# Kernel tuning notes

Measured on AMD Instinct MI355X. Metric: run time of the kernel, lower is better.

## Reference

```python
import jax, jax.numpy as jnp
import numpy as np

N = 100000
E = 1600000
IN_C, HID_C, OUT_C = 128, 128, 64
EPS = 1e-5


def setup_inputs() -> dict:
    key = jax.random.key(0)
    ks = jax.random.split(key, 12)
    x = jax.random.normal(ks[0], (N, IN_C), dtype=jnp.float32)
    edge_index = jax.random.randint(ks[1], (2, E), 0, N, dtype=jnp.int64)
    def lin(k, fan_in, fan_out):
        s = 1.0 / np.sqrt(fan_in)
        return jax.random.uniform(k, (fan_in, fan_out), jnp.float32, -s, s)
    return {
        "x": x,
        "W1": lin(ks[2], IN_C, HID_C), "b1": jnp.zeros((HID_C,), jnp.float32),
        "g1": jnp.ones((HID_C,), jnp.float32), "be1": jnp.zeros((HID_C,), jnp.float32),
        "W2": lin(ks[3], HID_C, HID_C), "b2": jnp.zeros((HID_C,), jnp.float32),
        "g2": jnp.ones((HID_C,), jnp.float32), "be2": jnp.zeros((HID_C,), jnp.float32),
        "W3": lin(ks[4], HID_C, OUT_C), "b3": jnp.zeros((OUT_C,), jnp.float32),
        "edge_index": edge_index,
    }


def gcn_conv(x, W, b, src, dst, dinv):
    # x' = D^{-1/2}(A+I)D^{-1/2} (x W) + b ; src/dst already include self loops
    h = x @ W                                    # [N, C_out]
    norm = dinv[src] * dinv[dst]                 # [E+N]
    msg = h[src] * norm[:, None]                 # [E+N, C_out] (memory-bound gather)
    out = jax.ops.segment_sum(msg, dst, num_segments=N)
    return out + b


def batchnorm_relu(h, gamma, beta):
    # training-mode BatchNorm1d: batch stats over nodes, biased variance
    mean = jnp.mean(h, axis=0)
    var = jnp.mean((h - mean) ** 2, axis=0)
    y = gamma * (h - mean) * jax.lax.rsqrt(var + EPS) + beta
    return jax.nn.relu(y)


def reference(x, W1, b1, g1, be1, W2, b2, g2, be2, W3, b3, edge_index):
    loop = jnp.arange(N, dtype=edge_index.dtype)
    src = jnp.concatenate([edge_index[0], loop])
    dst = jnp.concatenate([edge_index[1], loop])
    deg = jax.ops.segment_sum(jnp.ones_like(dst, dtype=jnp.float32), dst, num_segments=N)
    dinv = jax.lax.rsqrt(jnp.maximum(deg, 1.0))

    h = gcn_conv(x, W1, b1, src, dst, dinv)
    h = batchnorm_relu(h, g1, be1)
    h = gcn_conv(h, W2, b2, src, dst, dinv)
    h = batchnorm_relu(h, g2, be2)
    out = gcn_conv(h, W3, b3, src, dst, dinv)
    return (h, out)
```

## Files before the change

### kernel.cpp

```cpp
#include <hip/hip_runtime.h>
#include <hip/hip_bf16.h>

#define NNODES 100000
#define NEDGES 1600000
#define EPSBN 1e-5f

#define BKT_SHIFT 9
#define NODES_PER_BKT 512
#define NBKT 196
#define NCHUNK 256
#define CHUNK 6250
#define SRC_MASK 0x1FFFF
#define NSLOT 64

typedef unsigned short u16;
typedef unsigned int u32;
typedef __bf16 bf16x8 __attribute__((ext_vector_type(8)));
typedef float floatx4 __attribute__((ext_vector_type(4)));

__device__ __forceinline__ u16 f2bf(float f) {
    unsigned int u = __float_as_uint(f);
    unsigned int r = (u + 0x7fffu + ((u >> 16) & 1u)) >> 16;
    return (u16)r;
}
__device__ __forceinline__ float bflo(unsigned int u) { return __uint_as_float(u << 16); }
__device__ __forceinline__ float bfhi(unsigned int u) { return __uint_as_float(u & 0xffff0000u); }


__global__ __launch_bounds__(256) void k_hist(const int* __restrict__ ei, int* __restrict__ histT) {
    __shared__ int h[NBKT];
    int tid = threadIdx.x;
    if (tid < NBKT) h[tid] = 0;
    __syncthreads();
    int base = blockIdx.x * CHUNK;
    for (int e = base + tid; e < base + CHUNK; e += 256) {
        int d = ei[NEDGES + e];
        atomicAdd(&h[d >> BKT_SHIFT], 1);
    }
    __syncthreads();
    if (tid < NBKT) histT[tid * NCHUNK + blockIdx.x] = h[tid];
}

__global__ __launch_bounds__(256) void k_bbase(const int* __restrict__ histT, int* __restrict__ bbase,
                                               int* __restrict__ rowptr) {
    __shared__ int sdata[256];
    int tid = threadIdx.x;
    int s = 0;
    if (tid < NBKT) {
        for (int g = 0; g < NCHUNK; ++g) s += histT[tid * NCHUNK + g];
    }
    int val = s;
    sdata[tid] = val;
    __syncthreads();
    for (int off = 1; off < 256; off <<= 1) {
        int add = (tid >= off) ? sdata[tid - off] : 0;
        __syncthreads();
        val += add;
        sdata[tid] = val;
        __syncthreads();
    }
    if (tid < NBKT) bbase[tid] = val - s;
    if (tid == 0) { bbase[NBKT] = NEDGES; rowptr[NNODES] = NEDGES; }
}

__global__ __launch_bounds__(256) void k_bscan(const int* __restrict__ histT, const int* __restrict__ bbase,
                                               int* __restrict__ offT) {
    __shared__ int sdata[256];
    int b = blockIdx.x;
    int g = threadIdx.x;
    int v = histT[b * NCHUNK + g];
    int val = v;
    sdata[g] = val;
    __syncthreads();
    for (int off = 1; off < 256; off <<= 1) {
        int add = (g >= off) ? sdata[g - off] : 0;
        __syncthreads();
        val += add;
        sdata[g] = val;
        __syncthreads();
    }
    offT[b * NCHUNK + g] = bbase[b] + (val - v);
}

__global__ __launch_bounds__(256) void k_scatter(const int* __restrict__ ei, const int* __restrict__ offT,
                                                 u32* __restrict__ rec) {
    __shared__ int cur[NBKT];
    int tid = threadIdx.x;
    if (tid < NBKT) cur[tid] = offT[tid * NCHUNK + blockIdx.x];
    __syncthreads();
    int base = blockIdx.x * CHUNK;
    for (int e = base + tid; e < base + CHUNK; e += 256) {
        int s = ei[e];
        int d = ei[NEDGES + e];
        int b = d >> BKT_SHIFT;
        int p = atomicAdd(&cur[b], 1);
        rec[p] = ((u32)(d & (NODES_PER_BKT - 1)) << 17) | (u32)s;
    }
}

__global__ __launch_bounds__(256) void k_bfill(const u32* __restrict__ rec, const int* __restrict__ bbase,
                                               int* __restrict__ rowptr, float* __restrict__ dinv,
                                               int* __restrict__ colsrc) {
    __shared__ int cnt[NODES_PER_BKT];
    __shared__ int sdata[256];
    int tid = threadIdx.x;
    int b = blockIdx.x;
    int n0 = b * NODES_PER_BKT;
    int r0 = bbase[b], r1 = bbase[b + 1];
    cnt[2 * tid] = 0;
    cnt[2 * tid + 1] = 0;
    __syncthreads();
    for (int r = r0 + tid; r < r1; r += 256) {
        atomicAdd(&cnt[rec[r] >> 17], 1);
    }
    __syncthreads();
    int c0 = cnt[2 * tid], c1 = cnt[2 * tid + 1];
    int ps = c0 + c1;
    int val = ps;
    sdata[tid] = val;
    __syncthreads();
    for (int off = 1; off < 256; off <<= 1) {
        int add = (tid >= off) ? sdata[tid - off] : 0;
        __syncthreads();
        val += add;
        sdata[tid] = val;
        __syncthreads();
    }
    int e0 = val - ps;
    int e1 = e0 + c0;
    int na = n0 + 2 * tid, nb2 = n0 + 2 * tid + 1;
    if (na < NNODES) {
        rowptr[na] = r0 + e0;
        dinv[na] = rsqrtf((float)(c0 + 1));
    }
    if (nb2 < NNODES) {
        rowptr[nb2] = r0 + e1;
        dinv[nb2] = rsqrtf((float)(c1 + 1));
    }
    cnt[2 * tid] = r0 + e0;
    cnt[2 * tid + 1] = r0 + e1;
    __syncthreads();
    for (int r = r0 + tid; r < r1; r += 256) {
        u32 u = rec[r];
        int p = atomicAdd(&cnt[u >> 17], 1);
        colsrc[p] = (int)(u & SRC_MASK);
    }
}


template <int COUT>
__device__ __forceinline__ void packone(const float* __restrict__ W, u16* __restrict__ Wp, int f) {
    constexpr int CT = COUT / 16;
    if (f >= 4 * CT * 64) return;
    int ks = f / (CT * 64);
    int ct = (f / 64) % CT;
    int lane = f % 64;
    int quad = lane >> 4, mm = lane & 15;
#pragma unroll
    for (int j = 0; j < 8; ++j) {
        float v = W[(size_t)(ks * 32 + quad * 8 + j) * COUT + ct * 16 + mm];
        Wp[(size_t)f * 8 + j] = f2bf(v);
    }
}

__global__ __launch_bounds__(256) void k_packW_all(const float* __restrict__ W1, const float* __restrict__ W2,
                                                   const float* __restrict__ W3, u16* __restrict__ Wp1,
                                                   u16* __restrict__ Wp2, u16* __restrict__ Wp3) {
    int b = blockIdx.x;
    if (b < 8) packone<128>(W1, Wp1, b * 256 + threadIdx.x);
    else if (b < 16) packone<128>(W2, Wp2, (b - 8) * 256 + threadIdx.x);
    else packone<64>(W3, Wp3, (b - 16) * 256 + threadIdx.x);
}


template <int COUT, bool AFFINE, bool WRITEH>
__global__ __launch_bounds__(256) void k_mfma_gemm(const float* __restrict__ Xf, const u16* __restrict__ Wp,
                                                   const float* __restrict__ dinv,
                                                   const float* __restrict__ scale, const float* __restrict__ shift,
                                                   u16* __restrict__ Bout, float* __restrict__ Hout) {
    constexpr int CT = COUT / 16;
    const int wave = threadIdx.x >> 6;
    const int lane = threadIdx.x & 63;
    const int quad = lane >> 4;
    const int m = lane & 15;
    const int rowbase = blockIdx.x * 64 + wave * 16;
    const int arow = rowbase + m;
    const bool rv = arow < NNODES;
    floatx4 acc[CT];
#pragma unroll
    for (int ct = 0; ct < CT; ++ct) acc[ct] = floatx4{0.f, 0.f, 0.f, 0.f};
#pragma unroll
    for (int ks = 0; ks < 4; ++ks) {
        const int k0 = ks * 32 + quad * 8;
        float4 xa = make_float4(0.f, 0.f, 0.f, 0.f), xb = xa;
        if (rv) {
            xa = *(const float4*)(Xf + (size_t)arow * 128 + k0);
            xb = *(const float4*)(Xf + (size_t)arow * 128 + k0 + 4);
        }
        if (AFFINE) {
            float4 sa = *(const float4*)(scale + k0), sb = *(const float4*)(scale + k0 + 4);
            float4 ha = *(const float4*)(shift + k0), hb = *(const float4*)(shift + k0 + 4);
            xa.x = fmaxf(fmaf(xa.x, sa.x, ha.x), 0.f);
            xa.y = fmaxf(fmaf(xa.y, sa.y, ha.y), 0.f);
            xa.z = fmaxf(fmaf(xa.z, sa.z, ha.z), 0.f);
            xa.w = fmaxf(fmaf(xa.w, sa.w, ha.w), 0.f);
            xb.x = fmaxf(fmaf(xb.x, sb.x, hb.x), 0.f);
            xb.y = fmaxf(fmaf(xb.y, sb.y, hb.y), 0.f);
            xb.z = fmaxf(fmaf(xb.z, sb.z, hb.z), 0.f);
            xb.w = fmaxf(fmaf(xb.w, sb.w, hb.w), 0.f);
        }
        if (WRITEH && rv) {
            *(float4*)(Hout + (size_t)arow * 128 + k0) = xa;
            *(float4*)(Hout + (size_t)arow * 128 + k0 + 4) = xb;
        }
        union { u16 h[8]; bf16x8 v; } ua;
        ua.h[0] = f2bf(xa.x); ua.h[1] = f2bf(xa.y); ua.h[2] = f2bf(xa.z); ua.h[3] = f2bf(xa.w);
        ua.h[4] = f2bf(xb.x); ua.h[5] = f2bf(xb.y); ua.h[6] = f2bf(xb.z); ua.h[7] = f2bf(xb.w);
#pragma unroll
        for (int ct = 0; ct < CT; ++ct) {
            uint4 bv = *(const uint4*)(Wp + ((size_t)(ks * CT + ct) * 64 + lane) * 8);
            bf16x8 b = *(const bf16x8*)&bv;
            acc[ct] = __builtin_amdgcn_mfma_f32_16x16x32_bf16(ua.v, b, acc[ct], 0, 0, 0);
        }
    }
    float dv[4];
#pragma unroll
    for (int reg = 0; reg < 4; ++reg) {
        int r = rowbase + quad * 4 + reg;
        dv[reg] = (r < NNODES) ? dinv[r] : 0.f;
    }
#pragma unroll
    for (int ct = 0; ct < CT; ++ct) {
#pragma unroll
        for (int reg = 0; reg < 4; ++reg) {
            int r = rowbase + quad * 4 + reg;
            if (r < NNODES) Bout[(size_t)r * COUT + ct * 16 + m] = f2bf(dv[reg] * acc[ct][reg]);
        }
    }
}


template <bool STATS>
__global__ __launch_bounds__(256) void k_agg128v(const u16* __restrict__ Bm, const float* __restrict__ dinv,
                                                 const int* __restrict__ rowptr, const int* __restrict__ colsrc,
                                                 const float* __restrict__ bias, float* __restrict__ Out,
                                                 float* __restrict__ slots) {
    __shared__ float sO[4][128];
    const int wave = threadIdx.x >> 6;
    const int node = blockIdx.x * 4 + wave;
    const int lane = threadIdx.x & 63;
    const int g = lane >> 4;
    const int c16 = lane & 15;
    const uint4* Bq = (const uint4*)Bm;
    float a0[8], a1[8];
#pragma unroll
    for (int j = 0; j < 8; ++j) { a0[j] = 0.f; a1[j] = 0.f; }
    const int beg = rowptr[node];
    const int L = rowptr[node + 1] - beg + 1;
    for (int it = 0; it < L; it += 8) {
        int i0 = it + g, i1 = it + 4 + g;
        float w0 = (i0 < L) ? 1.f : 0.f;
        float w1 = (i1 < L) ? 1.f : 0.f;
        i0 = min(i0, L - 1);
        i1 = min(i1, L - 1);
        int s0 = colsrc[beg + max(i0, 1) - 1];
        int s1 = colsrc[beg + max(i1, 1) - 1];
        if (i0 == 0) s0 = node;
        uint4 q0 = Bq[(size_t)s0 * 16 + c16];
        uint4 q1 = Bq[(size_t)s1 * 16 + c16];
        a0[0] += w0 * bflo(q0.x); a0[1] += w0 * bfhi(q0.x);
        a0[2] += w0 * bflo(q0.y); a0[3] += w0 * bfhi(q0.y);
        a0[4] += w0 * bflo(q0.z); a0[5] += w0 * bfhi(q0.z);
        a0[6] += w0 * bflo(q0.w); a0[7] += w0 * bfhi(q0.w);
        a1[0] += w1 * bflo(q1.x); a1[1] += w1 * bfhi(q1.x);
        a1[2] += w1 * bflo(q1.y); a1[3] += w1 * bfhi(q1.y);
        a1[4] += w1 * bflo(q1.z); a1[5] += w1 * bfhi(q1.z);
        a1[6] += w1 * bflo(q1.w); a1[7] += w1 * bfhi(q1.w);
    }
    const float dv = dinv[node];
    float o[8];
#pragma unroll
    for (int j = 0; j < 8; ++j) {
        float s = a0[j] + a1[j];
        s += __shfl_xor(s, 16);
        s += __shfl_xor(s, 32);
        o[j] = dv * s + bias[c16 * 8 + j];
    }
    if (g == 0) {
        float4 v0 = make_float4(o[0], o[1], o[2], o[3]);
        float4 v1 = make_float4(o[4], o[5], o[6], o[7]);
        *(float4*)(Out + (size_t)node * 128 + c16 * 8) = v0;
        *(float4*)(Out + (size_t)node * 128 + c16 * 8 + 4) = v1;
        if (STATS) {
#pragma unroll
            for (int j = 0; j < 8; ++j) sO[wave][c16 * 8 + j] = o[j];
        }
    }
    if (STATS) {
        __syncthreads();
        if (threadIdx.x < 128) {
            float s = 0.f, q = 0.f;
#pragma unroll
            for (int wv = 0; wv < 4; ++wv) {
                float v = sO[wv][threadIdx.x];
                s += v;
                q += v * v;
            }
            float* slot = slots + (size_t)(blockIdx.x & (NSLOT - 1)) * 256;
            atomicAdd(&slot[threadIdx.x], s);
            atomicAdd(&slot[128 + threadIdx.x], q);
        }
    }
}

__global__ __launch_bounds__(256) void k_agg64v(const u16* __restrict__ Bm, const float* __restrict__ dinv,
                                                const int* __restrict__ rowptr, const int* __restrict__ colsrc,
                                                const float* __restrict__ bias, float* __restrict__ Out) {
    const int node = blockIdx.x * 4 + (threadIdx.x >> 6);
    const int lane = threadIdx.x & 63;
    const int g = lane >> 3;
    const int c8 = lane & 7;
    const uint4* Bq = (const uint4*)Bm;
    float a0[8], a1[8];
#pragma unroll
    for (int j = 0; j < 8; ++j) { a0[j] = 0.f; a1[j] = 0.f; }
    const int beg = rowptr[node];
    const int L = rowptr[node + 1] - beg + 1;
    for (int it = 0; it < L; it += 16) {
        int i0 = it + g, i1 = it + 8 + g;
        float w0 = (i0 < L) ? 1.f : 0.f;
        float w1 = (i1 < L) ? 1.f : 0.f;
        i0 = min(i0, L - 1);
        i1 = min(i1, L - 1);
        int s0 = colsrc[beg + max(i0, 1) - 1];
        int s1 = colsrc[beg + max(i1, 1) - 1];
        if (i0 == 0) s0 = node;
        uint4 q0 = Bq[(size_t)s0 * 8 + c8];
        uint4 q1 = Bq[(size_t)s1 * 8 + c8];
        a0[0] += w0 * bflo(q0.x); a0[1] += w0 * bfhi(q0.x);
        a0[2] += w0 * bflo(q0.y); a0[3] += w0 * bfhi(q0.y);
        a0[4] += w0 * bflo(q0.z); a0[5] += w0 * bfhi(q0.z);
        a0[6] += w0 * bflo(q0.w); a0[7] += w0 * bfhi(q0.w);
        a1[0] += w1 * bflo(q1.x); a1[1] += w1 * bfhi(q1.x);
        a1[2] += w1 * bflo(q1.y); a1[3] += w1 * bfhi(q1.y);
        a1[4] += w1 * bflo(q1.z); a1[5] += w1 * bfhi(q1.z);
        a1[6] += w1 * bflo(q1.w); a1[7] += w1 * bfhi(q1.w);
    }
    const float dv = dinv[node];
    float o[8];
#pragma unroll
    for (int j = 0; j < 8; ++j) {
        float s = a0[j] + a1[j];
        s += __shfl_xor(s, 8);
        s += __shfl_xor(s, 16);
        s += __shfl_xor(s, 32);
        o[j] = dv * s + bias[c8 * 8 + j];
    }
    if (g == 0) {
        float4 v0 = make_float4(o[0], o[1], o[2], o[3]);
        float4 v1 = make_float4(o[4], o[5], o[6], o[7]);
        *(float4*)(Out + (size_t)node * 64 + c8 * 8) = v0;
        *(float4*)(Out + (size_t)node * 64 + c8 * 8 + 4) = v1;
    }
}


__global__ void k_bn_final(const float* __restrict__ slots, const float* __restrict__ g,
                           const float* __restrict__ be, float* __restrict__ scale, float* __restrict__ shift) {
    int c = threadIdx.x;
    float s = 0.f, q = 0.f;
    for (int k = 0; k < NSLOT; ++k) {
        s += slots[(size_t)k * 256 + c];
        q += slots[(size_t)k * 256 + 128 + c];
    }
    float mean = s * (1.0f / NNODES);
    float var = q * (1.0f / NNODES) - mean * mean;
    float istd = rsqrtf(var + EPSBN);
    float sc = g[c] * istd;
    scale[c] = sc;
    shift[c] = be[c] - sc * mean;
}


extern "C" void kernel_launch(void* const* d_in, const int* in_sizes, int n_in,
                              void* d_out, int out_size, void* d_ws, size_t ws_size,
                              hipStream_t stream) {
    const float* x   = (const float*)d_in[0];
    const float* W1  = (const float*)d_in[1];
    const float* b1  = (const float*)d_in[2];
    const float* g1  = (const float*)d_in[3];
    const float* be1 = (const float*)d_in[4];
    const float* W2  = (const float*)d_in[5];
    const float* b2  = (const float*)d_in[6];
    const float* g2  = (const float*)d_in[7];
    const float* be2 = (const float*)d_in[8];
    const float* W3  = (const float*)d_in[9];
    const float* b3  = (const float*)d_in[10];
    const int* ei    = (const int*)d_in[11];

    float* out_h = (float*)d_out;
    float* out_o = (float*)d_out + (size_t)NNODES * 128;

    char* w = (char*)d_ws;
    float* A = (float*)w;      w += (size_t)NNODES * 128 * 4;
    u16* Bm = (u16*)w;         w += (size_t)NNODES * 128 * 2;
    float* dinv = (float*)w;   w += (size_t)NNODES * 4;
    int* rowptr = (int*)w;     w += (size_t)(NNODES + 32) * 4;
    int* colsrc = (int*)w;     w += (size_t)(NEDGES + 8) * 4;
    int* bbase = (int*)w;      w += (NBKT + 4) * 4;
    float* slots1 = (float*)w; w += (size_t)NSLOT * 256 * 4;
    float* slots2 = (float*)w; w += (size_t)NSLOT * 256 * 4;
    float* scale = (float*)w;  w += 128 * 4;
    float* shift = (float*)w;  w += 128 * 4;
    u16* Wp1 = (u16*)w;        w += 128 * 128 * 2;
    u16* Wp2 = (u16*)w;        w += 128 * 128 * 2;
    u16* Wp3 = (u16*)w;        w += 128 * 64 * 2;

    u32* rec  = (u32*)A;
    int* histT = (int*)Bm;
    int* offT  = (int*)Bm + NBKT * NCHUNK;

    hipMemsetAsync(slots1, 0, (size_t)2 * NSLOT * 256 * 4, stream);

    k_packW_all<<<20, 256, 0, stream>>>(W1, W2, W3, Wp1, Wp2, Wp3);

    k_hist<<<NCHUNK, 256, 0, stream>>>(ei, histT);
    k_bbase<<<1, 256, 0, stream>>>(histT, bbase, rowptr);
    k_bscan<<<NBKT, 256, 0, stream>>>(histT, bbase, offT);
    k_scatter<<<NCHUNK, 256, 0, stream>>>(ei, offT, rec);
    k_bfill<<<NBKT, 256, 0, stream>>>(rec, bbase, rowptr, dinv, colsrc);

    const int GB = (NNODES + 63) / 64;
    const int AB = NNODES / 4;

    k_mfma_gemm<128, false, false><<<GB, 256, 0, stream>>>(x, Wp1, dinv, nullptr, nullptr, Bm, nullptr);
    k_agg128v<true><<<AB, 256, 0, stream>>>(Bm, dinv, rowptr, colsrc, b1, A, slots1);
    k_bn_final<<<1, 128, 0, stream>>>(slots1, g1, be1, scale, shift);

    k_mfma_gemm<128, true, false><<<GB, 256, 0, stream>>>(A, Wp2, dinv, scale, shift, Bm, nullptr);
    k_agg128v<true><<<AB, 256, 0, stream>>>(Bm, dinv, rowptr, colsrc, b2, A, slots2);
    k_bn_final<<<1, 128, 0, stream>>>(slots2, g2, be2, scale, shift);

    k_mfma_gemm<64, true, true><<<GB, 256, 0, stream>>>(A, Wp3, dinv, scale, shift, Bm, out_h);
    k_agg64v<<<AB, 256, 0, stream>>>(Bm, dinv, rowptr, colsrc, b3, out_o);
}
```

Before: 460.4 us.

## Slab-partition features into 16-channel slabs so aggregation gathers fit in cache

The GEMM writes its bf16 output in a channel-slab layout of 16 channels by all nodes. The aggregation kernels now run one block per (node group, slab), so each gather pass touches only one slab of about 3.2 MB that can stay cache-resident. Intermediate activations are now stored as bf16 slabs instead of fp32, which halves their traffic. BN stats now use per-node atomics rather than a per-block shared-memory reduction, which adds more atomic contention, and the extra bf16 rounding of activations changes precision.

```diff
diff --git a/kernel.cpp b/kernel.cpp
--- a/kernel.cpp
+++ b/kernel.cpp
@@ -173,8 +173,8 @@
 }
 
 
-template <int COUT, bool AFFINE, bool WRITEH>
-__global__ __launch_bounds__(256) void k_mfma_gemm(const float* __restrict__ Xf, const u16* __restrict__ Wp,
+template <int COUT, bool BF16A, bool AFFINE, bool WRITEH>
+__global__ __launch_bounds__(256) void k_mfma_gemm(const void* __restrict__ Xin, const u16* __restrict__ Wp,
                                                    const float* __restrict__ dinv,
                                                    const float* __restrict__ scale, const float* __restrict__ shift,
                                                    u16* __restrict__ Bout, float* __restrict__ Hout) {
@@ -192,30 +192,45 @@
 #pragma unroll
     for (int ks = 0; ks < 4; ++ks) {
         const int k0 = ks * 32 + quad * 8;
-        float4 xa = make_float4(0.f, 0.f, 0.f, 0.f), xb = xa;
-        if (rv) {
-            xa = *(const float4*)(Xf + (size_t)arow * 128 + k0);
-            xb = *(const float4*)(Xf + (size_t)arow * 128 + k0 + 4);
+        float xv[8];
+        if (BF16A) {
+            uint4 q = make_uint4(0u, 0u, 0u, 0u);
+            if (rv) {
+                const u16* base = (const u16*)Xin + ((size_t)((k0 >> 4) * NNODES + arow)) * 16 + (k0 & 15);
+                q = *(const uint4*)base;
+            }
+            xv[0] = bflo(q.x); xv[1] = bfhi(q.x);
+            xv[2] = bflo(q.y); xv[3] = bfhi(q.y);
+            xv[4] = bflo(q.z); xv[5] = bfhi(q.z);
+            xv[6] = bflo(q.w); xv[7] = bfhi(q.w);
+        } else {
+            float4 xa = make_float4(0.f, 0.f, 0.f, 0.f), xb = xa;
+            if (rv) {
+                xa = *(const float4*)((const float*)Xin + (size_t)arow * 128 + k0);
+                xb = *(const float4*)((const float*)Xin + (size_t)arow * 128 + k0 + 4);
+            }
+            xv[0] = xa.x; xv[1] = xa.y; xv[2] = xa.z; xv[3] = xa.w;
+            xv[4] = xb.x; xv[5] = xb.y; xv[6] = xb.z; xv[7] = xb.w;
         }
         if (AFFINE) {
             float4 sa = *(const float4*)(scale + k0), sb = *(const float4*)(scale + k0 + 4);
             float4 ha = *(const float4*)(shift + k0), hb = *(const float4*)(shift + k0 + 4);
-            xa.x = fmaxf(fmaf(xa.x, sa.x, ha.x), 0.f);
-            xa.y = fmaxf(fmaf(xa.y, sa.y, ha.y), 0.f);
-            xa.z = fmaxf(fmaf(xa.z, sa.z, ha.z), 0.f);
-            xa.w = fmaxf(fmaf(xa.w, sa.w, ha.w), 0.f);
-            xb.x = fmaxf(fmaf(xb.x, sb.x, hb.x), 0.f);
-            xb.y = fmaxf(fmaf(xb.y, sb.y, hb.y), 0.f);
-            xb.z = fmaxf(fmaf(xb.z, sb.z, hb.z), 0.f);
-            xb.w = fmaxf(fmaf(xb.w, sb.w, hb.w), 0.f);
+            xv[0] = fmaxf(fmaf(xv[0], sa.x, ha.x), 0.f);
+            xv[1] = fmaxf(fmaf(xv[1], sa.y, ha.y), 0.f);
+            xv[2] = fmaxf(fmaf(xv[2], sa.z, ha.z), 0.f);
+            xv[3] = fmaxf(fmaf(xv[3], sa.w, ha.w), 0.f);
+            xv[4] = fmaxf(fmaf(xv[4], sb.x, hb.x), 0.f);
+            xv[5] = fmaxf(fmaf(xv[5], sb.y, hb.y), 0.f);
+            xv[6] = fmaxf(fmaf(xv[6], sb.z, hb.z), 0.f);
+            xv[7] = fmaxf(fmaf(xv[7], sb.w, hb.w), 0.f);
         }
         if (WRITEH && rv) {
-            *(float4*)(Hout + (size_t)arow * 128 + k0) = xa;
-            *(float4*)(Hout + (size_t)arow * 128 + k0 + 4) = xb;
+            *(float4*)(Hout + (size_t)arow * 128 + k0) = make_float4(xv[0], xv[1], xv[2], xv[3]);
+            *(float4*)(Hout + (size_t)arow * 128 + k0 + 4) = make_float4(xv[4], xv[5], xv[6], xv[7]);
         }
         union { u16 h[8]; bf16x8 v; } ua;
-        ua.h[0] = f2bf(xa.x); ua.h[1] = f2bf(xa.y); ua.h[2] = f2bf(xa.z); ua.h[3] = f2bf(xa.w);
-        ua.h[4] = f2bf(xb.x); ua.h[5] = f2bf(xb.y); ua.h[6] = f2bf(xb.z); ua.h[7] = f2bf(xb.w);
+#pragma unroll
+        for (int j = 0; j < 8; ++j) ua.h[j] = f2bf(xv[j]);
 #pragma unroll
         for (int ct = 0; ct < CT; ++ct) {
             uint4 bv = *(const uint4*)(Wp + ((size_t)(ks * CT + ct) * 64 + lane) * 8);
@@ -234,133 +249,107 @@
 #pragma unroll
         for (int reg = 0; reg < 4; ++reg) {
             int r = rowbase + quad * 4 + reg;
-            if (r < NNODES) Bout[(size_t)r * COUT + ct * 16 + m] = f2bf(dv[reg] * acc[ct][reg]);
+            if (r < NNODES) Bout[((size_t)(ct * NNODES + r)) * 16 + m] = f2bf(dv[reg] * acc[ct][reg]);
         }
     }
 }
 
 
 template <bool STATS>
-__global__ __launch_bounds__(256) void k_agg128v(const u16* __restrict__ Bm, const float* __restrict__ dinv,
+__global__ __launch_bounds__(256) void k_aggs128(const u16* __restrict__ Bs, const float* __restrict__ dinv,
                                                  const int* __restrict__ rowptr, const int* __restrict__ colsrc,
-                                                 const float* __restrict__ bias, float* __restrict__ Out,
+                                                 const float* __restrict__ bias, u16* __restrict__ As,
                                                  float* __restrict__ slots) {
-    __shared__ float sO[4][128];
+    const int slab = blockIdx.x & 7;
     const int wave = threadIdx.x >> 6;
-    const int node = blockIdx.x * 4 + wave;
-    const int lane = threadIdx.x & 63;
-    const int g = lane >> 4;
-    const int c16 = lane & 15;
-    const uint4* Bq = (const uint4*)Bm;
-    float a0[8], a1[8];
-#pragma unroll
-    for (int j = 0; j < 8; ++j) { a0[j] = 0.f; a1[j] = 0.f; }
-    const int beg = rowptr[node];
-    const int L = rowptr[node + 1] - beg + 1;
-    for (int it = 0; it < L; it += 8) {
-        int i0 = it + g, i1 = it + 4 + g;
-        float w0 = (i0 < L) ? 1.f : 0.f;
-        float w1 = (i1 < L) ? 1.f : 0.f;
-        i0 = min(i0, L - 1);
-        i1 = min(i1, L - 1);
-        int s0 = colsrc[beg + max(i0, 1) - 1];
-        int s1 = colsrc[beg + max(i1, 1) - 1];
-        if (i0 == 0) s0 = node;
-        uint4 q0 = Bq[(size_t)s0 * 16 + c16];
-        uint4 q1 = Bq[(size_t)s1 * 16 + c16];
-        a0[0] += w0 * bflo(q0.x); a0[1] += w0 * bfhi(q0.x);
-        a0[2] += w0 * bflo(q0.y); a0[3] += w0 * bfhi(q0.y);
-        a0[4] += w0 * bflo(q0.z); a0[5] += w0 * bfhi(q0.z);
-        a0[6] += w0 * bflo(q0.w); a0[7] += w0 * bfhi(q0.w);
-        a1[0] += w1 * bflo(q1.x); a1[1] += w1 * bfhi(q1.x);
-        a1[2] += w1 * bflo(q1.y); a1[3] += w1 * bfhi(q1.y);
-        a1[4] += w1 * bflo(q1.z); a1[5] += w1 * bfhi(q1.z);
-        a1[6] += w1 * bflo(q1.w); a1[7] += w1 * bfhi(q1.w);
-    }
-    const float dv = dinv[node];
-    float o[8];
-#pragma unroll
-    for (int j = 0; j < 8; ++j) {
-        float s = a0[j] + a1[j];
-        s += __shfl_xor(s, 16);
-        s += __shfl_xor(s, 32);
-        o[j] = dv * s + bias[c16 * 8 + j];
-    }
-    if (g == 0) {
-        float4 v0 = make_float4(o[0], o[1], o[2], o[3]);
-        float4 v1 = make_float4(o[4], o[5], o[6], o[7]);
-        *(float4*)(Out + (size_t)node * 128 + c16 * 8) = v0;
-        *(float4*)(Out + (size_t)node * 128 + c16 * 8 + 4) = v1;
-        if (STATS) {
-#pragma unroll
-            for (int j = 0; j < 8; ++j) sO[wave][c16 * 8 + j] = o[j];
-        }
-    }
-    if (STATS) {
-        __syncthreads();
-        if (threadIdx.x < 128) {
-            float s = 0.f, q = 0.f;
-#pragma unroll
-            for (int wv = 0; wv < 4; ++wv) {
-                float v = sO[wv][threadIdx.x];
-                s += v;
-                q += v * v;
-            }
-            float* slot = slots + (size_t)(blockIdx.x & (NSLOT - 1)) * 256;
-            atomicAdd(&slot[threadIdx.x], s);
-            atomicAdd(&slot[128 + threadIdx.x], q);
-        }
-    }
-}
-
-__global__ __launch_bounds__(256) void k_agg64v(const u16* __restrict__ Bm, const float* __restrict__ dinv,
-                                                const int* __restrict__ rowptr, const int* __restrict__ colsrc,
-                                                const float* __restrict__ bias, float* __restrict__ Out) {
-    const int node = blockIdx.x * 4 + (threadIdx.x >> 6);
+    const int node = (blockIdx.x >> 3) * 4 + wave;
     const int lane = threadIdx.x & 63;
     const int g = lane >> 3;
     const int c8 = lane & 7;
-    const uint4* Bq = (const uint4*)Bm;
-    float a0[8], a1[8];
-#pragma unroll
-    for (int j = 0; j < 8; ++j) { a0[j] = 0.f; a1[j] = 0.f; }
+    const u32* B = (const u32*)Bs + (size_t)slab * NNODES * 8;
     const int beg = rowptr[node];
     const int L = rowptr[node + 1] - beg + 1;
+    float a0 = 0.f, a1 = 0.f, b0 = 0.f, b1 = 0.f;
     for (int it = 0; it < L; it += 16) {
         int i0 = it + g, i1 = it + 8 + g;
         float w0 = (i0 < L) ? 1.f : 0.f;
         float w1 = (i1 < L) ? 1.f : 0.f;
         i0 = min(i0, L - 1);
         i1 = min(i1, L - 1);
-        int s0 = colsrc[beg + max(i0, 1) - 1];
-        int s1 = colsrc[beg + max(i1, 1) - 1];
+        int x0 = min(beg + max(i0, 1) - 1, NEDGES - 1);
+        int x1 = min(beg + max(i1, 1) - 1, NEDGES - 1);
+        int s0 = colsrc[x0];
+        int s1 = colsrc[x1];
         if (i0 == 0) s0 = node;
-        uint4 q0 = Bq[(size_t)s0 * 8 + c8];
-        uint4 q1 = Bq[(size_t)s1 * 8 + c8];
-        a0[0] += w0 * bflo(q0.x); a0[1] += w0 * bfhi(q0.x);
-        a0[2] += w0 * bflo(q0.y); a0[3] += w0 * bfhi(q0.y);
-        a0[4] += w0 * bflo(q0.z); a0[5] += w0 * bfhi(q0.z);
-        a0[6] += w0 * bflo(q0.w); a0[7] += w0 * bfhi(q0.w);
-        a1[0] += w1 * bflo(q1.x); a1[1] += w1 * bfhi(q1.x);
-        a1[2] += w1 * bflo(q1.y); a1[3] += w1 * bfhi(q1.y);
-        a1[4] += w1 * bflo(q1.z); a1[5] += w1 * bfhi(q1.z);
-        a1[6] += w1 * bflo(q1.w); a1[7] += w1 * bfhi(q1.w);
-    }
-    const float dv = dinv[node];
-    float o[8];
-#pragma unroll
-    for (int j = 0; j < 8; ++j) {
-        float s = a0[j] + a1[j];
-        s += __shfl_xor(s, 8);
-        s += __shfl_xor(s, 16);
-        s += __shfl_xor(s, 32);
-        o[j] = dv * s + bias[c8 * 8 + j];
-    }
+        if (i1 == 0) s1 = node;
+        u32 q0 = B[(size_t)s0 * 8 + c8];
+        u32 q1 = B[(size_t)s1 * 8 + c8];
+        a0 += w0 * bflo(q0); a1 += w0 * bfhi(q0);
+        b0 += w1 * bflo(q1); b1 += w1 * bfhi(q1);
+    }
+    a0 += b0; a1 += b1;
+    a0 += __shfl_xor(a0, 8);  a1 += __shfl_xor(a1, 8);
+    a0 += __shfl_xor(a0, 16); a1 += __shfl_xor(a1, 16);
+    a0 += __shfl_xor(a0, 32); a1 += __shfl_xor(a1, 32);
     if (g == 0) {
-        float4 v0 = make_float4(o[0], o[1], o[2], o[3]);
-        float4 v1 = make_float4(o[4], o[5], o[6], o[7]);
-        *(float4*)(Out + (size_t)node * 64 + c8 * 8) = v0;
-        *(float4*)(Out + (size_t)node * 64 + c8 * 8 + 4) = v1;
+        const float dv = dinv[node];
+        const int ch = slab * 16 + 2 * c8;
+        float o0 = dv * a0 + bias[ch];
+        float o1 = dv * a1 + bias[ch + 1];
+        ((u32*)As)[((size_t)(slab * NNODES + node)) * 8 + c8] = (u32)f2bf(o0) | ((u32)f2bf(o1) << 16);
+        if (STATS) {
+            float* slot = slots + (size_t)(node & (NSLOT - 1)) * 256;
+            atomicAdd(&slot[ch], o0);
+            atomicAdd(&slot[ch + 1], o1);
+            atomicAdd(&slot[128 + ch], o0 * o0);
+            atomicAdd(&slot[128 + ch + 1], o1 * o1);
+        }
+    }
+}
+
+__global__ __launch_bounds__(256) void k_aggs64(const u16* __restrict__ Bs, const float* __restrict__ dinv,
+                                                const int* __restrict__ rowptr, const int* __restrict__ colsrc,
+                                                const float* __restrict__ bias, float* __restrict__ Out) {
+    const int cls = blockIdx.x & 7;
+    const int slab = cls >> 1;
+    const int half = cls & 1;
+    const int wave = threadIdx.x >> 6;
+    const int node = (blockIdx.x >> 3) * 4 + wave + half * (NNODES / 2);
+    const int lane = threadIdx.x & 63;
+    const int g = lane >> 3;
+    const int c8 = lane & 7;
+    const u32* B = (const u32*)Bs + (size_t)slab * NNODES * 8;
+    const int beg = rowptr[node];
+    const int L = rowptr[node + 1] - beg + 1;
+    float a0 = 0.f, a1 = 0.f, b0 = 0.f, b1 = 0.f;
+    for (int it = 0; it < L; it += 16) {
+        int i0 = it + g, i1 = it + 8 + g;
+        float w0 = (i0 < L) ? 1.f : 0.f;
+        float w1 = (i1 < L) ? 1.f : 0.f;
+        i0 = min(i0, L - 1);
+        i1 = min(i1, L - 1);
+        int x0 = min(beg + max(i0, 1) - 1, NEDGES - 1);
+        int x1 = min(beg + max(i1, 1) - 1, NEDGES - 1);
+        int s0 = colsrc[x0];
+        int s1 = colsrc[x1];
+        if (i0 == 0) s0 = node;
+        if (i1 == 0) s1 = node;
+        u32 q0 = B[(size_t)s0 * 8 + c8];
+        u32 q1 = B[(size_t)s1 * 8 + c8];
+        a0 += w0 * bflo(q0); a1 += w0 * bfhi(q0);
+        b0 += w1 * bflo(q1); b1 += w1 * bfhi(q1);
+    }
+    a0 += b0; a1 += b1;
+    a0 += __shfl_xor(a0, 8);  a1 += __shfl_xor(a1, 8);
+    a0 += __shfl_xor(a0, 16); a1 += __shfl_xor(a1, 16);
+    a0 += __shfl_xor(a0, 32); a1 += __shfl_xor(a1, 32);
+    if (g == 0) {
+        const float dv = dinv[node];
+        const int ch = slab * 16 + 2 * c8;
+        float2 o;
+        o.x = dv * a0 + bias[ch];
+        o.y = dv * a1 + bias[ch + 1];
+        *(float2*)(Out + (size_t)node * 64 + ch) = o;
     }
 }
 
@@ -402,7 +391,7 @@
     float* out_o = (float*)d_out + (size_t)NNODES * 128;
 
     char* w = (char*)d_ws;
-    float* A = (float*)w;      w += (size_t)NNODES * 128 * 4;
+    u16* As = (u16*)w;         w += (size_t)NNODES * 128 * 2;
     u16* Bm = (u16*)w;         w += (size_t)NNODES * 128 * 2;
     float* dinv = (float*)w;   w += (size_t)NNODES * 4;
     int* rowptr = (int*)w;     w += (size_t)(NNODES + 32) * 4;
@@ -416,7 +405,7 @@
     u16* Wp2 = (u16*)w;        w += 128 * 128 * 2;
     u16* Wp3 = (u16*)w;        w += 128 * 64 * 2;
 
-    u32* rec  = (u32*)A;
+    u32* rec  = (u32*)As;
     int* histT = (int*)Bm;
     int* offT  = (int*)Bm + NBKT * NCHUNK;
 
@@ -431,16 +420,17 @@
     k_bfill<<<NBKT, 256, 0, stream>>>(rec, bbase, rowptr, dinv, colsrc);
 
     const int GB = (NNODES + 63) / 64;
-    const int AB = NNODES / 4;
-
-    k_mfma_gemm<128, false, false><<<GB, 256, 0, stream>>>(x, Wp1, dinv, nullptr, nullptr, Bm, nullptr);
-    k_agg128v<true><<<AB, 256, 0, stream>>>(Bm, dinv, rowptr, colsrc, b1, A, slots1);
+    const int AB128 = (NNODES / 4) * 8;
+    const int AB64 = (NNODES / 8) * 8;
+
+    k_mfma_gemm<128, false, false, false><<<GB, 256, 0, stream>>>(x, Wp1, dinv, nullptr, nullptr, Bm, nullptr);
+    k_aggs128<true><<<AB128, 256, 0, stream>>>(Bm, dinv, rowptr, colsrc, b1, As, slots1);
     k_bn_final<<<1, 128, 0, stream>>>(slots1, g1, be1, scale, shift);
 
-    k_mfma_gemm<128, true, false><<<GB, 256, 0, stream>>>(A, Wp2, dinv, scale, shift, Bm, nullptr);
-    k_agg128v<true><<<AB, 256, 0, stream>>>(Bm, dinv, rowptr, colsrc, b2, A, slots2);
+    k_mfma_gemm<128, true, true, false><<<GB, 256, 0, stream>>>(As, Wp2, dinv, scale, shift, Bm, nullptr);
+    k_aggs128<true><<<AB128, 256, 0, stream>>>(Bm, dinv, rowptr, colsrc, b2, As, slots2);
     k_bn_final<<<1, 128, 0, stream>>>(slots2, g2, be2, scale, shift);
 
-    k_mfma_gemm<64, true, true><<<GB, 256, 0, stream>>>(A, Wp3, dinv, scale, shift, Bm, out_h);
-    k_agg64v<<<AB, 256, 0, stream>>>(Bm, dinv, rowptr, colsrc, b3, out_o);
-}
+    k_mfma_gemm<64, true, true, true><<<GB, 256, 0, stream>>>(As, Wp3, dinv, scale, shift, Bm, out_h);
+    k_aggs64<<<AB64, 256, 0, stream>>>(Bm, dinv, rowptr, colsrc, b3, out_o);
+}
```

New measurement: 968.6 us. 110% more time.
